# Kernel tuning notes

Measured on AMD Instinct MI355X. Metric: run time of the kernel, lower is better.

Reference implementation:

```python
import jax, jax.numpy as jnp
import numpy as np

H = W = 128          # render resolution
TS = 4               # texture_size from the module
DIST, ELEV, AZIM = 2.732, 0.0, 90.0   # camera (azimuth fixed for determinism)
BIG = 1e10


def setup_inputs() -> dict:
    key = jax.random.key(0)
    # UV-sphere mesh (stands in for nr.load_obj)
    nlat, nlon = 33, 40
    theta = np.linspace(0.15, np.pi - 0.15, nlat)
    phi = np.linspace(0.0, 2.0 * np.pi, nlon, endpoint=False)
    tt, pp = np.meshgrid(theta, phi, indexing='ij')
    verts = np.stack([np.sin(tt) * np.cos(pp), np.cos(tt), np.sin(tt) * np.sin(pp)], -1)
    verts = verts.reshape(-1, 3).astype(np.float32)          # [V,3]
    idx = lambda i, j: i * nlon + (j % nlon)
    faces = []
    for i in range(nlat - 1):
        for j in range(nlon):
            faces.append([idx(i, j), idx(i + 1, j), idx(i, j + 1)])
            faces.append([idx(i, j + 1), idx(i + 1, j), idx(i + 1, j + 1)])
    faces = np.asarray(faces, np.int32)                       # [F,3], F=2560
    k1, k2 = jax.random.split(key)
    textures = 0.1 * jax.random.normal(k1, (1, faces.shape[0], TS, TS, TS, 3), jnp.float32)
    image_ref = jax.random.uniform(k2, (1, 3, H, W), jnp.float32)
    return {
        'vertices': jnp.asarray(verts)[None],                 # [1,V,3]
        'textures': textures,                                 # [1,F,4,4,4,3]
        'image_ref': image_ref,                               # [1,3,H,W]
        'faces': jnp.asarray(faces)[None],                    # [1,F,3] int32
    }


def _look_at(v, eye):
    # neural_renderer look_at: at=origin, up=+y
    up = jnp.array([0.0, 1.0, 0.0], v.dtype)
    z = -eye / jnp.linalg.norm(eye)
    x = jnp.cross(up, z); x = x / jnp.linalg.norm(x)
    y = jnp.cross(z, x)
    R = jnp.stack([x, y, z])                                  # rows: camera axes
    return (v - eye) @ R.T


def _edge(a, b, p):
    # signed area cross product; a,b: [...,2], p broadcastable [...,2]
    return (b[..., 0] - a[..., 0]) * (p[..., 1] - a[..., 1]) - \
           (b[..., 1] - a[..., 1]) * (p[..., 0] - a[..., 0])


def reference(vertices, textures, image_ref, faces):
    el, az = jnp.deg2rad(ELEV), jnp.deg2rad(AZIM)
    eye = DIST * jnp.array([jnp.cos(el) * jnp.sin(az), jnp.sin(el), -jnp.cos(el) * jnp.cos(az)])

    v = _look_at(vertices[0], eye)                            # [V,3] camera space
    tri = v[faces[0]]                                         # [F,3,3]
    p2 = tri[..., :2]                                         # orthographic proj [F,3,2]
    z3 = tri[..., 2]                                          # [F,3]

    xs = (jnp.arange(W, dtype=jnp.float32) + 0.5) / W * 2.0 - 1.0
    ys = 1.0 - (jnp.arange(H, dtype=jnp.float32) + 0.5) / H * 2.0
    gy, gx = jnp.meshgrid(ys, xs, indexing='ij')
    px = jnp.stack([gx.ravel(), gy.ravel()], -1)              # [P,2]
    P = px.shape[0]

    a, b, c = p2[:, 0], p2[:, 1], p2[:, 2]                    # [F,2]
    area = _edge(a, b, c)                                     # [F]
    sa = jnp.where(jnp.abs(area) < 1e-8, 1e-8, area)
    pb = px[:, None, :]                                       # [P,1,2]
    w0 = _edge(b, c, pb) / sa                                 # [P,F]
    w1 = _edge(c, a, pb) / sa
    w2 = _edge(a, b, pb) / sa
    inside = (w0 >= 0) & (w1 >= 0) & (w2 >= 0) & (jnp.abs(area) >= 1e-8)
    depth = w0 * z3[:, 0] + w1 * z3[:, 1] + w2 * z3[:, 2]     # [P,F]
    zbuf = jnp.where(inside, depth, BIG)
    fidx = jnp.argmin(zbuf, axis=1)                           # [P] winning face
    hit = jnp.min(zbuf, axis=1) < BIG * 0.5                   # [P]

    # recompute barycentric only for the winning face (grads flow here)
    tw = p2[fidx]                                             # [P,3,2]
    zw = z3[fidx]                                             # [P,3]
    aw, bw, cw = tw[:, 0], tw[:, 1], tw[:, 2]
    arw = _edge(aw, bw, cw)
    srw = jnp.where(jnp.abs(arw) < 1e-8, 1e-8, arw)
    u0 = _edge(bw, cw, px) / srw
    u1 = _edge(cw, aw, px) / srw
    u2 = _edge(aw, bw, px) / srw
    w = jnp.clip(jnp.stack([u0, u1, u2], -1), 0.0, 1.0)       # [P,3]
    w = w / (jnp.sum(w, -1, keepdims=True) + 1e-8)

    # trilinear sample from per-face texture cube (ambient=1, directional=0)
    tex = jnp.tanh(textures)[0]                               # [F,TS,TS,TS,3]
    texf = tex[fidx]                                          # [P,TS,TS,TS,3]
    pos = w * (TS - 1)                                        # [P,3]
    lo = jnp.clip(jnp.floor(pos).astype(jnp.int32), 0, TS - 2)
    fr = pos - lo.astype(pos.dtype)                           # [P,3]
    pid = jnp.arange(P)
    col = jnp.zeros((P, 3), tex.dtype)
    for di in (0, 1):
        for dj in (0, 1):
            for dk in (0, 1):
                wgt = (fr[:, 0] if di else 1.0 - fr[:, 0]) * \
                      (fr[:, 1] if dj else 1.0 - fr[:, 1]) * \
                      (fr[:, 2] if dk else 1.0 - fr[:, 2])
                corner = texf[pid, lo[:, 0] + di, lo[:, 1] + dj, lo[:, 2] + dk]
                col = col + wgt[:, None] * corner

    flat = jnp.where(hit[:, None], col, 0.0)                  # [P,3]
    image = flat.reshape(H, W, 3).transpose(2, 0, 1)[None]    # [1,3,H,W]
    loss = jnp.sum((image - image_ref) ** 2)
    return loss
```

## Files before the change

kernel.cpp:

```cpp
#include <hip/hip_runtime.h>
#include <cmath>

#define H_ 128
#define W_ 128
#define P_ (H_ * W_)
#define NTX 16
#define NTY 16
#define NTILES (NTX * NTY)
#define CAP 512

struct Cam {
    float ex, ey, ez;
    float r00, r01, r02, r10, r11, r12, r20, r21, r22;
};

__global__ __launch_bounds__(256) void prep_faces(
    const float* __restrict__ verts, const int* __restrict__ faces,
    int F, Cam cam, float4* __restrict__ rec, int* __restrict__ bbox) {
#pragma clang fp contract(off)
    int f = blockIdx.x * blockDim.x + threadIdx.x;
    if (f >= F) return;
    float tx[3], ty[3], tz[3];
    for (int k = 0; k < 3; ++k) {
        int vi = faces[f * 3 + k];
        float vx = verts[vi * 3 + 0];
        float vy = verts[vi * 3 + 1];
        float vz = verts[vi * 3 + 2];
        float dx = vx - cam.ex, dy = vy - cam.ey, dz = vz - cam.ez;
        tx[k] = (dx * cam.r00 + dy * cam.r01) + dz * cam.r02;
        ty[k] = (dx * cam.r10 + dy * cam.r11) + dz * cam.r12;
        tz[k] = (dx * cam.r20 + dy * cam.r21) + dz * cam.r22;
    }
    float a0 = tx[0], a1 = ty[0], b0 = tx[1], b1 = ty[1], c0 = tx[2], c1 = ty[2];
    float area = (b0 - a0) * (c1 - a1) - (b1 - a1) * (c0 - a0);
    float ab = fabsf(area);
    float sa = (ab < 1e-8f) ? 1e-8f : area;
    float valid = (ab >= 1e-8f) ? 1.0f : 0.0f;
    rec[f * 3 + 0] = make_float4(a0, a1, b0, b1);
    rec[f * 3 + 1] = make_float4(c0, c1, tz[0], tz[1]);
    rec[f * 3 + 2] = make_float4(tz[2], sa, valid, 0.0f);

    int bb = -1;
    if (valid != 0.0f) {
        float minx = fminf(fminf(a0, b0), c0), maxx = fmaxf(fmaxf(a0, b0), c0);
        float miny = fminf(fminf(a1, b1), c1), maxy = fmaxf(fmaxf(a1, b1), c1);
        int colmin = (int)ceilf((minx + 1.0f) * 64.0f - 0.5f) - 1;
        int colmax = (int)floorf((maxx + 1.0f) * 64.0f - 0.5f) + 1;
        int rowmin = (int)ceilf((1.0f - maxy) * 64.0f - 0.5f) - 1;
        int rowmax = (int)floorf((1.0f - miny) * 64.0f - 0.5f) + 1;
        colmin = max(colmin, 0); colmax = min(colmax, W_ - 1);
        rowmin = max(rowmin, 0); rowmax = min(rowmax, H_ - 1);
        if (colmin <= colmax && rowmin <= rowmax) {
            bb = (colmin >> 3) | ((colmax >> 3) << 4)
               | ((rowmin >> 3) << 8) | ((rowmax >> 3) << 12);
        }
    }
    bbox[f] = bb;
}

__global__ __launch_bounds__(512) void raster_shade(
    const float4* __restrict__ rec, const float* __restrict__ tex,
    const float* __restrict__ ref, const int* __restrict__ bbox, int F,
    double* __restrict__ partials) {
#pragma clang fp contract(off)
    __shared__ int lcnt;
    __shared__ int lfi[CAP];
    __shared__ float4 lrec[CAP * 3];
    __shared__ unsigned long long lbest[8 * 64];
    int t = blockIdx.x;
    int tid = threadIdx.x;
    int mytx = t & (NTX - 1), myty = t >> 4;
    if (tid == 0) lcnt = 0;
    __syncthreads();
    for (int f = tid; f < F; f += 512) {
        int bb = bbox[f];
        if (bb < 0) continue;
        int tx0 = bb & 15, tx1 = (bb >> 4) & 15;
        int ty0 = (bb >> 8) & 15, ty1 = (bb >> 12) & 15;
        if (mytx >= tx0 && mytx <= tx1 && myty >= ty0 && myty <= ty1) {
            int slot = atomicAdd(&lcnt, 1);
            if (slot < CAP) lfi[slot] = f;
        }
    }
    __syncthreads();
    int n = min(lcnt, CAP);
    for (int j = tid; j < n; j += 512) {
        int f = lfi[j];
        lrec[j * 3 + 0] = rec[f * 3 + 0];
        lrec[j * 3 + 1] = rec[f * 3 + 1];
        lrec[j * 3 + 2] = rec[f * 3 + 2];
    }
    __syncthreads();

    int wv = tid >> 6, lane = tid & 63;
    int lx = lane & 7, ly = lane >> 3;
    int col = mytx * 8 + lx, row = myty * 8 + ly;
    int pid = row * W_ + col;
    float px = ((col + 0.5f) / 128.0f) * 2.0f - 1.0f;
    float py = 1.0f - ((row + 0.5f) / 128.0f) * 2.0f;
    unsigned long long best = ~0ull;
    for (int i = wv; i < n; i += 8) {
        float4 r0 = lrec[i * 3 + 0];
        float4 r1 = lrec[i * 3 + 1];
        float4 r2 = lrec[i * 3 + 2];
        float a0 = r0.x, a1 = r0.y, b0 = r0.z, b1 = r0.w;
        float c0 = r1.x, c1 = r1.y, z0 = r1.z, z1 = r1.w;
        float z2 = r2.x, sa = r2.y;
        float w0n = (c0 - b0) * (py - b1) - (c1 - b1) * (px - b0);
        float w1n = (a0 - c0) * (py - c1) - (a1 - c1) * (px - c0);
        float w2n = (b0 - a0) * (py - a1) - (b1 - a1) * (px - a0);
        bool ins;
        if (sa > 0.0f) ins = (w0n >= 0.0f) & (w1n >= 0.0f) & (w2n >= 0.0f);
        else           ins = (w0n <= 0.0f) & (w1n <= 0.0f) & (w2n <= 0.0f);
        if (ins) {
            float w0 = w0n / sa, w1 = w1n / sa, w2 = w2n / sa;
            float d = (w0 * z0 + w1 * z1) + w2 * z2;
            unsigned long long key =
                ((unsigned long long)__float_as_uint(d) << 32)
                | (unsigned)lfi[i];
            best = min(best, key);
        }
    }
    lbest[wv * 64 + lane] = best;
    __syncthreads();
    if (wv != 0) return;

    unsigned long long key = best;
    for (int s = 1; s < 8; ++s) key = min(key, lbest[s * 64 + lane]);
    float bd = __uint_as_float((unsigned)(key >> 32));
    bool hit = bd < 5e9f;
    int bestf = hit ? (int)(unsigned)(key & 0xffffffffu) : 0;
    float4 r0 = rec[bestf * 3 + 0];
    float4 r1 = rec[bestf * 3 + 1];
    float4 r2 = rec[bestf * 3 + 2];
    float a0 = r0.x, a1 = r0.y, b0 = r0.z, b1 = r0.w;
    float c0 = r1.x, c1 = r1.y, sa = r2.y;
    float u0 = ((c0 - b0) * (py - b1) - (c1 - b1) * (px - b0)) / sa;
    float u1 = ((a0 - c0) * (py - c1) - (a1 - c1) * (px - c0)) / sa;
    float u2 = ((b0 - a0) * (py - a1) - (b1 - a1) * (px - a0)) / sa;
    float w0 = fminf(fmaxf(u0, 0.0f), 1.0f);
    float w1 = fminf(fmaxf(u1, 0.0f), 1.0f);
    float w2 = fminf(fmaxf(u2, 0.0f), 1.0f);
    float ssum = ((w0 + w1) + w2) + 1e-8f;
    float n0 = w0 / ssum, n1 = w1 / ssum, n2 = w2 / ssum;
    float p0 = n0 * 3.0f, p1 = n1 * 3.0f, p2 = n2 * 3.0f;
    int l0 = (int)floorf(p0); l0 = min(max(l0, 0), 2);
    int l1 = (int)floorf(p1); l1 = min(max(l1, 0), 2);
    int l2 = (int)floorf(p2); l2 = min(max(l2, 0), 2);
    float fr0 = p0 - (float)l0;
    float fr1 = p1 - (float)l1;
    float fr2 = p2 - (float)l2;
    const float* tb = tex + (size_t)bestf * 192;
    float cr = 0.0f, cg = 0.0f, cb = 0.0f;
    for (int di = 0; di < 2; ++di)
        for (int dj = 0; dj < 2; ++dj)
            for (int dk = 0; dk < 2; ++dk) {
                float wx = di ? fr0 : (1.0f - fr0);
                float wy = dj ? fr1 : (1.0f - fr1);
                float wz = dk ? fr2 : (1.0f - fr2);
                float wgt = (wx * wy) * wz;
                int off = (((l0 + di) * 4 + (l1 + dj)) * 4 + (l2 + dk)) * 3;
                cr = cr + wgt * tanhf(tb[off + 0]);
                cg = cg + wgt * tanhf(tb[off + 1]);
                cb = cb + wgt * tanhf(tb[off + 2]);
            }
    double acc = 0.0;
    {
        float fc = hit ? cr : 0.0f;
        float d = fc - ref[0 * P_ + pid];
        acc += (double)(d * d);
        fc = hit ? cg : 0.0f;
        d = fc - ref[1 * P_ + pid];
        acc += (double)(d * d);
        fc = hit ? cb : 0.0f;
        d = fc - ref[2 * P_ + pid];
        acc += (double)(d * d);
    }
    for (int off = 32; off > 0; off >>= 1) acc += __shfl_down(acc, off);
    if (lane == 0) partials[t] = acc;
}

__global__ __launch_bounds__(64) void finalize(
    const double* __restrict__ partials, float* __restrict__ out) {
    double v = 0.0;
    for (int k = 0; k < 4; ++k) v += partials[threadIdx.x * 4 + k];
    for (int off = 32; off > 0; off >>= 1) v += __shfl_xor(v, off);
    if (threadIdx.x == 0) out[0] = (float)v;
}

extern "C" void kernel_launch(void* const* d_in, const int* in_sizes, int n_in,
                              void* d_out, int out_size, void* d_ws, size_t ws_size,
                              hipStream_t stream) {
    const float* vertices = (const float*)d_in[0];
    const float* textures = (const float*)d_in[1];
    const float* image_ref = (const float*)d_in[2];
    const int* faces = (const int*)d_in[3];
    int F = in_sizes[3] / 3;

    float az = (float)(90.0 * M_PI / 180.0);
    float el = 0.0f;
    float ce = cosf(el), se = sinf(el);
    float sz = sinf(az), cz = cosf(az);
    const float DIST = 2.732f;
    float ex = DIST * (ce * sz);
    float ey = DIST * se;
    float ez = DIST * (-(ce * cz));
    float nrm = sqrtf((ex * ex + ey * ey) + ez * ez);
    float z0 = -ex / nrm, z1 = -ey / nrm, z2 = -ez / nrm;
    float x0 = 1.0f * z2 - 0.0f * z1;
    float x1 = 0.0f * z0 - 0.0f * z2;
    float x2 = 0.0f * z1 - 1.0f * z0;
    float xn = sqrtf((x0 * x0 + x1 * x1) + x2 * x2);
    x0 /= xn; x1 /= xn; x2 /= xn;
    float y0 = z1 * x2 - z2 * x1;
    float y1 = z2 * x0 - z0 * x2;
    float y2 = z0 * x1 - z1 * x0;
    Cam cam{ex, ey, ez, x0, x1, x2, y0, y1, y2, z0, z1, z2};

    size_t recB = ((size_t)F * 48 + 255) & ~(size_t)255;
    size_t bbB = ((size_t)F * sizeof(int) + 255) & ~(size_t)255;
    float4* rec = (float4*)d_ws;
    int* bbox = (int*)((char*)d_ws + recB);
    double* partials = (double*)((char*)d_ws + recB + bbB);

    hipLaunchKernelGGL(prep_faces, dim3((F + 255) / 256), dim3(256), 0, stream,
                       vertices, faces, F, cam, rec, bbox);
    hipLaunchKernelGGL(raster_shade, dim3(NTILES), dim3(512), 0, stream,
                       rec, textures, image_ref, bbox, F, partials);
    hipLaunchKernelGGL(finalize, dim3(1), dim3(64), 0, stream,
                       partials, (float*)d_out);
}
```

Measured before the change: 22.04 us.

## Fuse face preprocessing into raster kernel, recomputing projections per tile

Removes the separate prep_faces kernel. Each tile block now projects every face itself, culls it against its own tile bounds, and writes the surviving face records straight into shared memory. The shading stage recomputes the winning face's projection from the vertices instead of reading a stored record. This drops one kernel launch and the global round trip for the records and bounding boxes, at the cost of every one of the 256 blocks redoing the projection of all 2560 faces with gathered vertex loads.

```diff
diff --git a/kernel.cpp b/kernel.cpp
--- a/kernel.cpp
+++ b/kernel.cpp
@@ -14,53 +14,9 @@
     float r00, r01, r02, r10, r11, r12, r20, r21, r22;
 };
 
-__global__ __launch_bounds__(256) void prep_faces(
-    const float* __restrict__ verts, const int* __restrict__ faces,
-    int F, Cam cam, float4* __restrict__ rec, int* __restrict__ bbox) {
-#pragma clang fp contract(off)
-    int f = blockIdx.x * blockDim.x + threadIdx.x;
-    if (f >= F) return;
-    float tx[3], ty[3], tz[3];
-    for (int k = 0; k < 3; ++k) {
-        int vi = faces[f * 3 + k];
-        float vx = verts[vi * 3 + 0];
-        float vy = verts[vi * 3 + 1];
-        float vz = verts[vi * 3 + 2];
-        float dx = vx - cam.ex, dy = vy - cam.ey, dz = vz - cam.ez;
-        tx[k] = (dx * cam.r00 + dy * cam.r01) + dz * cam.r02;
-        ty[k] = (dx * cam.r10 + dy * cam.r11) + dz * cam.r12;
-        tz[k] = (dx * cam.r20 + dy * cam.r21) + dz * cam.r22;
-    }
-    float a0 = tx[0], a1 = ty[0], b0 = tx[1], b1 = ty[1], c0 = tx[2], c1 = ty[2];
-    float area = (b0 - a0) * (c1 - a1) - (b1 - a1) * (c0 - a0);
-    float ab = fabsf(area);
-    float sa = (ab < 1e-8f) ? 1e-8f : area;
-    float valid = (ab >= 1e-8f) ? 1.0f : 0.0f;
-    rec[f * 3 + 0] = make_float4(a0, a1, b0, b1);
-    rec[f * 3 + 1] = make_float4(c0, c1, tz[0], tz[1]);
-    rec[f * 3 + 2] = make_float4(tz[2], sa, valid, 0.0f);
-
-    int bb = -1;
-    if (valid != 0.0f) {
-        float minx = fminf(fminf(a0, b0), c0), maxx = fmaxf(fmaxf(a0, b0), c0);
-        float miny = fminf(fminf(a1, b1), c1), maxy = fmaxf(fmaxf(a1, b1), c1);
-        int colmin = (int)ceilf((minx + 1.0f) * 64.0f - 0.5f) - 1;
-        int colmax = (int)floorf((maxx + 1.0f) * 64.0f - 0.5f) + 1;
-        int rowmin = (int)ceilf((1.0f - maxy) * 64.0f - 0.5f) - 1;
-        int rowmax = (int)floorf((1.0f - miny) * 64.0f - 0.5f) + 1;
-        colmin = max(colmin, 0); colmax = min(colmax, W_ - 1);
-        rowmin = max(rowmin, 0); rowmax = min(rowmax, H_ - 1);
-        if (colmin <= colmax && rowmin <= rowmax) {
-            bb = (colmin >> 3) | ((colmax >> 3) << 4)
-               | ((rowmin >> 3) << 8) | ((rowmax >> 3) << 12);
-        }
-    }
-    bbox[f] = bb;
-}
-
-__global__ __launch_bounds__(512) void raster_shade(
-    const float4* __restrict__ rec, const float* __restrict__ tex,
-    const float* __restrict__ ref, const int* __restrict__ bbox, int F,
+__global__ __launch_bounds__(512) void render_all(
+    const float* __restrict__ verts, const int* __restrict__ faces, int F,
+    Cam cam, const float* __restrict__ tex, const float* __restrict__ ref,
     double* __restrict__ partials) {
 #pragma clang fp contract(off)
     __shared__ int lcnt;
@@ -72,25 +28,46 @@
     int mytx = t & (NTX - 1), myty = t >> 4;
     if (tid == 0) lcnt = 0;
     __syncthreads();
+
     for (int f = tid; f < F; f += 512) {
-        int bb = bbox[f];
-        if (bb < 0) continue;
-        int tx0 = bb & 15, tx1 = (bb >> 4) & 15;
-        int ty0 = (bb >> 8) & 15, ty1 = (bb >> 12) & 15;
-        if (mytx >= tx0 && mytx <= tx1 && myty >= ty0 && myty <= ty1) {
-            int slot = atomicAdd(&lcnt, 1);
-            if (slot < CAP) lfi[slot] = f;
+        float tx[3], ty[3], tz[3];
+        for (int k = 0; k < 3; ++k) {
+            int vi = faces[f * 3 + k];
+            float vx = verts[vi * 3 + 0];
+            float vy = verts[vi * 3 + 1];
+            float vz = verts[vi * 3 + 2];
+            float dx = vx - cam.ex, dy = vy - cam.ey, dz = vz - cam.ez;
+            tx[k] = (dx * cam.r00 + dy * cam.r01) + dz * cam.r02;
+            ty[k] = (dx * cam.r10 + dy * cam.r11) + dz * cam.r12;
+            tz[k] = (dx * cam.r20 + dy * cam.r21) + dz * cam.r22;
+        }
+        float a0 = tx[0], a1 = ty[0], b0 = tx[1], b1 = ty[1];
+        float c0 = tx[2], c1 = ty[2];
+        float area = (b0 - a0) * (c1 - a1) - (b1 - a1) * (c0 - a0);
+        float ab = fabsf(area);
+        if (ab < 1e-8f) continue;
+        float sa = area;
+        float minx = fminf(fminf(a0, b0), c0), maxx = fmaxf(fmaxf(a0, b0), c0);
+        float miny = fminf(fminf(a1, b1), c1), maxy = fmaxf(fmaxf(a1, b1), c1);
+        int colmin = (int)ceilf((minx + 1.0f) * 64.0f - 0.5f) - 1;
+        int colmax = (int)floorf((maxx + 1.0f) * 64.0f - 0.5f) + 1;
+        int rowmin = (int)ceilf((1.0f - maxy) * 64.0f - 0.5f) - 1;
+        int rowmax = (int)floorf((1.0f - miny) * 64.0f - 0.5f) + 1;
+        colmin = max(colmin, 0); colmax = min(colmax, W_ - 1);
+        rowmin = max(rowmin, 0); rowmax = min(rowmax, H_ - 1);
+        if (colmin > colmax || rowmin > rowmax) continue;
+        if (mytx < (colmin >> 3) || mytx > (colmax >> 3) ||
+            myty < (rowmin >> 3) || myty > (rowmax >> 3)) continue;
+        int slot = atomicAdd(&lcnt, 1);
+        if (slot < CAP) {
+            lfi[slot] = f;
+            lrec[slot * 3 + 0] = make_float4(a0, a1, b0, b1);
+            lrec[slot * 3 + 1] = make_float4(c0, c1, tz[0], tz[1]);
+            lrec[slot * 3 + 2] = make_float4(tz[2], sa, 0.0f, 0.0f);
         }
     }
     __syncthreads();
     int n = min(lcnt, CAP);
-    for (int j = tid; j < n; j += 512) {
-        int f = lfi[j];
-        lrec[j * 3 + 0] = rec[f * 3 + 0];
-        lrec[j * 3 + 1] = rec[f * 3 + 1];
-        lrec[j * 3 + 2] = rec[f * 3 + 2];
-    }
-    __syncthreads();
 
     int wv = tid >> 6, lane = tid & 63;
     int lx = lane & 7, ly = lane >> 3;
@@ -130,11 +107,22 @@
     float bd = __uint_as_float((unsigned)(key >> 32));
     bool hit = bd < 5e9f;
     int bestf = hit ? (int)(unsigned)(key & 0xffffffffu) : 0;
-    float4 r0 = rec[bestf * 3 + 0];
-    float4 r1 = rec[bestf * 3 + 1];
-    float4 r2 = rec[bestf * 3 + 2];
-    float a0 = r0.x, a1 = r0.y, b0 = r0.z, b1 = r0.w;
-    float c0 = r1.x, c1 = r1.y, sa = r2.y;
+    float a0, a1, b0, b1, c0, c1, sa;
+    {
+        float tx[3], ty[3];
+        for (int k = 0; k < 3; ++k) {
+            int vi = faces[bestf * 3 + k];
+            float vx = verts[vi * 3 + 0];
+            float vy = verts[vi * 3 + 1];
+            float vz = verts[vi * 3 + 2];
+            float dx = vx - cam.ex, dy = vy - cam.ey, dz = vz - cam.ez;
+            tx[k] = (dx * cam.r00 + dy * cam.r01) + dz * cam.r02;
+            ty[k] = (dx * cam.r10 + dy * cam.r11) + dz * cam.r12;
+        }
+        a0 = tx[0]; a1 = ty[0]; b0 = tx[1]; b1 = ty[1]; c0 = tx[2]; c1 = ty[2];
+        float area = (b0 - a0) * (c1 - a1) - (b1 - a1) * (c0 - a0);
+        sa = (fabsf(area) < 1e-8f) ? 1e-8f : area;
+    }
     float u0 = ((c0 - b0) * (py - b1) - (c1 - b1) * (px - b0)) / sa;
     float u1 = ((a0 - c0) * (py - c1) - (a1 - c1) * (px - c0)) / sa;
     float u2 = ((b0 - a0) * (py - a1) - (b1 - a1) * (px - a0)) / sa;
@@ -217,16 +205,10 @@
     float y2 = z0 * x1 - z1 * x0;
     Cam cam{ex, ey, ez, x0, x1, x2, y0, y1, y2, z0, z1, z2};
 
-    size_t recB = ((size_t)F * 48 + 255) & ~(size_t)255;
-    size_t bbB = ((size_t)F * sizeof(int) + 255) & ~(size_t)255;
-    float4* rec = (float4*)d_ws;
-    int* bbox = (int*)((char*)d_ws + recB);
-    double* partials = (double*)((char*)d_ws + recB + bbB);
-
-    hipLaunchKernelGGL(prep_faces, dim3((F + 255) / 256), dim3(256), 0, stream,
-                       vertices, faces, F, cam, rec, bbox);
-    hipLaunchKernelGGL(raster_shade, dim3(NTILES), dim3(512), 0, stream,
-                       rec, textures, image_ref, bbox, F, partials);
+    double* partials = (double*)d_ws;
+
+    hipLaunchKernelGGL(render_all, dim3(NTILES), dim3(512), 0, stream,
+                       vertices, faces, F, cam, textures, image_ref, partials);
     hipLaunchKernelGGL(finalize, dim3(1), dim3(64), 0, stream,
                        partials, (float*)d_out);
 }
```

Measured after the change: 18.16 us. -17.6%, faster.
